# Performance work log

Hardware: AMD Instinct MI355X
Metric: run time of the kernel (lower is better)

## Reference

```python
import jax, jax.numpy as jnp
import numpy as np
import math

B, S, D, H = 4, 2048, 1024, 16
DEPTH = D // H


def setup_inputs() -> dict:
    key = jax.random.key(0)
    ks = jax.random.split(key, 8)
    scale = 1.0 / math.sqrt(D)
    return {
        "v": jax.random.normal(ks[0], (B, S, D), dtype=jnp.float32),
        "k": jax.random.normal(ks[1], (B, S, D), dtype=jnp.float32),
        "q": jax.random.normal(ks[2], (B, S, D), dtype=jnp.float32),
        "wq_w": jax.random.normal(ks[3], (D, D), dtype=jnp.float32) * scale,
        "wq_b": jnp.zeros((D,), dtype=jnp.float32),
        "wk_w": jax.random.normal(ks[4], (D, D), dtype=jnp.float32) * scale,
        "wk_b": jnp.zeros((D,), dtype=jnp.float32),
        "wv_w": jax.random.normal(ks[5], (D, D), dtype=jnp.float32) * scale,
        "wv_b": jnp.zeros((D,), dtype=jnp.float32),
        "dense_w": jax.random.normal(ks[6], (D, D), dtype=jnp.float32) * scale,
        "dense_b": jnp.zeros((D,), dtype=jnp.float32),
    }


def _split_heads(x):
    # [B, S, D] -> [B, H, S, depth]
    b, s, _ = x.shape
    return x.reshape(b, s, H, DEPTH).transpose(0, 2, 1, 3)


def reference(v, k, q, wq_w, wq_b, wk_w, wk_b, wv_w, wv_b, dense_w, dense_b):
    # Linear projections (torch Linear: x @ W.T + b)
    qh = _split_heads(q @ wq_w.T + wq_b)
    kh = _split_heads(k @ wk_w.T + wk_b)
    vh = _split_heads(v @ wv_w.T + wv_b)

    # scaled dot-product attention; scores: [B, H, S, S]
    scores = jnp.einsum("bhqd,bhkd->bhqk", qh, kh) / math.sqrt(DEPTH)
    attn = jax.nn.softmax(scores, axis=-1)
    ctx = jnp.einsum("bhqk,bhkd->bhqd", attn, vh)

    # merge heads: [B, H, S, depth] -> [B, S, D]
    ctx = ctx.transpose(0, 2, 1, 3).reshape(q.shape[0], -1, D)
    return ctx @ dense_w.T + dense_b
```

## Files before the change

### kernel.cpp

```cpp
#include <hip/hip_runtime.h>
#include <hip/hip_bf16.h>
#include <stdint.h>

#define B_  4
#define S_  2048
#define D_  1024
#define H_  16
#define DP_ 64
#define M_  (B_*S_)

typedef __bf16 bf16x8 __attribute__((ext_vector_type(8)));
typedef __bf16 bf16x2_t __attribute__((ext_vector_type(2)));
typedef float  f32x4  __attribute__((ext_vector_type(4)));
typedef float  f32x16 __attribute__((ext_vector_type(16)));
typedef float  f32x2_t __attribute__((ext_vector_type(2)));
typedef unsigned short u16x8 __attribute__((ext_vector_type(8)));

__device__ __forceinline__ unsigned short f2bf(float f) {
    __bf16 b = (__bf16)f;
    return __builtin_bit_cast(unsigned short, b);
}
__device__ __forceinline__ unsigned pk_bf16(float lo, float hi) {
    f32x2_t f = {lo, hi};
    bf16x2_t b = __builtin_convertvector(f, bf16x2_t);
    return __builtin_bit_cast(unsigned, b);
}
__device__ __forceinline__ bf16x8 ld_frag(const unsigned short* p) {
    return __builtin_bit_cast(bf16x8, *(const u16x8*)p);
}
__device__ __forceinline__ f32x4 mfma16(bf16x8 a, bf16x8 b, f32x4 c) {
    return __builtin_amdgcn_mfma_f32_16x16x32_bf16(a, b, c, 0, 0, 0);
}
__device__ __forceinline__ f32x16 mfma32(bf16x8 a, bf16x8 b, f32x16 c) {
    return __builtin_amdgcn_mfma_f32_32x32x16_bf16(a, b, c, 0, 0, 0);
}
__device__ __forceinline__ void pl32swap(unsigned &a, unsigned &b) {
    asm volatile("v_permlane32_swap_b32 %0, %1" : "+v"(a), "+v"(b));
}
__device__ __forceinline__ void gl2lds16(const void* g, void* l) {
    __builtin_amdgcn_global_load_lds(
        (const __attribute__((address_space(1))) unsigned*)g,
        (__attribute__((address_space(3))) unsigned*)l, 16, 0, 0);
}

__global__ __launch_bounds__(256)
void cvt_all(const float* __restrict__ w0, const float* __restrict__ w1,
             const float* __restrict__ w2, const float* __restrict__ w3,
             const float* __restrict__ a0, const float* __restrict__ a1,
             const float* __restrict__ a2,
             unsigned short* __restrict__ Wcat, unsigned short* __restrict__ Acat)
{
    const int gid = blockIdx.x * 256 + threadIdx.x;
    const float* src; unsigned short* dst;
    if (gid < 524288) {
        const int wi = gid >> 17;
        const size_t off = (size_t)(gid & 131071) * 8;
        const float* ws[4] = {w0, w1, w2, w3};
        src = ws[wi] + off; dst = Wcat + (size_t)wi * 1048576 + off;
    } else {
        const int g2 = gid - 524288;
        const int ai = g2 >> 20;
        const size_t off = (size_t)(g2 & 1048575) * 8;
        const float* as[3] = {a0, a1, a2};
        src = as[ai] + off; dst = Acat + (size_t)ai * 8388608 + off;
    }
    float4 x = ((const float4*)src)[0];
    float4 y = ((const float4*)src)[1];
    uint4 o;
    o.x = pk_bf16(x.x, x.y); o.y = pk_bf16(x.z, x.w);
    o.z = pk_bf16(y.x, y.y); o.w = pk_bf16(y.z, y.w);
    *(uint4*)dst = o;
}

template<int MODE>
__global__ __launch_bounds__(256, 3)
void gemm_bt(const unsigned short* __restrict__ Acat, size_t a_stride,
             const unsigned short* __restrict__ Wcat,
             const float* __restrict__ bias0, const float* __restrict__ bias1,
             void* __restrict__ Out)
{
    __shared__ __align__(16) unsigned short SM[16384];
    unsigned short* As = SM;
    unsigned short* Bs = SM + 8192;

    const int z = (MODE == 1) ? blockIdx.z : 0;
    const unsigned short* A = Acat + (size_t)z * a_stride;
    const unsigned short* W = Wcat + ((size_t)z << 20);
    const float* bias = (z == 0) ? bias0 : bias1;

    const int tid  = threadIdx.x;
    const int wave = tid >> 6, lane = tid & 63;
    const int quad = lane >> 4, l16 = lane & 15;
    const int wm = (wave >> 1) * 64, wn = (wave & 1) * 64;
    const int row0 = blockIdx.x * 128, col0 = blockIdx.y * 128;

    const int srow = lane >> 3;
    const int sg   = (lane & 7) ^ srow;

    f32x4 acc[4][4];
#pragma unroll
    for (int i = 0; i < 4; i++)
#pragma unroll
        for (int j = 0; j < 4; j++) acc[i][j] = (f32x4){0.f, 0.f, 0.f, 0.f};

    auto stage = [&](int kt) {
        const int k0 = kt * 64;
#pragma unroll
        for (int j = 0; j < 4; ++j) {
            const int c = wave * 4 + j;
            gl2lds16(A + (size_t)(row0 + c * 8 + srow) * D_ + k0 + sg * 8,
                     (unsigned char*)As + c * 1024);
            gl2lds16(W + (size_t)(col0 + c * 8 + srow) * D_ + k0 + sg * 8,
                     (unsigned char*)Bs + c * 1024);
        }
    };

    stage(0);
    for (int kt = 0; kt < D_ / 64; ++kt) {
        __syncthreads();
        bf16x8 af[4][2], bv[4][2];
#pragma unroll
        for (int mi = 0; mi < 4; ++mi) {
            const int row = wm + mi * 16 + l16;
#pragma unroll
            for (int kd = 0; kd < 2; ++kd)
                af[mi][kd] = ld_frag(&As[row * 64 + (((kd * 4 + quad) ^ (row & 7)) * 8)]);
        }
#pragma unroll
        for (int ni = 0; ni < 4; ++ni) {
            const int row = wn + ni * 16 + l16;
#pragma unroll
            for (int kd = 0; kd < 2; ++kd)
                bv[ni][kd] = ld_frag(&Bs[row * 64 + (((kd * 4 + quad) ^ (row & 7)) * 8)]);
        }
        if (kt + 1 < D_ / 64) {
            __syncthreads();
            stage(kt + 1);
        }
#pragma unroll
        for (int kd = 0; kd < 2; ++kd)
#pragma unroll
            for (int mi = 0; mi < 4; ++mi)
#pragma unroll
                for (int ni = 0; ni < 4; ++ni) {
                    if (MODE == 1)
                        acc[mi][ni] = mfma16(bv[ni][kd], af[mi][kd], acc[mi][ni]);
                    else
                        acc[mi][ni] = mfma16(af[mi][kd], bv[ni][kd], acc[mi][ni]);
                }
    }

    if constexpr (MODE == 1) {
        unsigned short* Lt = SM;
        unsigned short* OutQK = (unsigned short*)Out + ((size_t)z << 23);
        const int bidx = row0 >> 11;
        const float scale = (z == 0) ? 0.18033688f : 1.0f;
#pragma unroll
        for (int hc = 0; hc < 2; ++hc) {
            __syncthreads();
            if ((wave & 1) == hc) {
#pragma unroll
                for (int ni = 0; ni < 4; ++ni) {
                    const int c_loc = wn + ni * 16 + quad * 4;
                    const float4 bb = *(const float4*)&bias[col0 + c_loc];
#pragma unroll
                    for (int mi = 0; mi < 4; ++mi) {
                        const int s_loc = wm + mi * 16 + l16;
                        uint2 w;
                        w.x = pk_bf16((acc[mi][ni][0] + bb.x) * scale,
                                      (acc[mi][ni][1] + bb.y) * scale);
                        w.y = pk_bf16((acc[mi][ni][2] + bb.z) * scale,
                                      (acc[mi][ni][3] + bb.w) * scale);
                        *(uint2*)&Lt[s_loc * 72 + (c_loc & 63)] = w;
                    }
                }
            }
            __syncthreads();
            const int hg = (col0 >> 6) + hc;
            const size_t qb = (size_t)(bidx * H_ + hg) * S_ + (row0 & (S_ - 1));
#pragma unroll
            for (int p = 0; p < 4; ++p) {
                const int s = p * 32 + (tid >> 3);
                const int g = tid & 7;
                uint4 d = *(const uint4*)&Lt[s * 72 + g * 8];
                *(uint4*)(OutQK + (qb + s) * DP_ + g * 8) = d;
            }
        }
        return;
    }
    if constexpr (MODE == 2) {
        unsigned short* Lt = SM;
        unsigned short* OutV = (unsigned short*)Out;
        const int bidx = row0 >> 11;
#pragma unroll
        for (int hc = 0; hc < 2; ++hc) {
            __syncthreads();
            if ((wave & 1) == hc) {
#pragma unroll
                for (int ni = 0; ni < 4; ++ni) {
                    const float bvv = bias0[col0 + hc * 64 + ni * 16 + l16];
#pragma unroll
                    for (int mi = 0; mi < 4; ++mi) {
                        uint2 w;
                        w.x = pk_bf16(acc[mi][ni][0] + bvv, acc[mi][ni][1] + bvv);
                        w.y = pk_bf16(acc[mi][ni][2] + bvv, acc[mi][ni][3] + bvv);
                        *(uint2*)&Lt[(ni * 16 + l16) * 132 + wm + mi * 16 + quad * 4] = w;
                    }
                }
            }
            __syncthreads();
            const int hg = (col0 >> 6) + hc;
            const size_t vb = ((size_t)(bidx * H_ + hg) * DP_) * S_;
#pragma unroll
            for (int p = 0; p < 4; ++p) {
                const int dpl = p * 16 + (tid >> 4);
                uint4 d = *(const uint4*)&Lt[dpl * 132 + (tid & 15) * 8];
                *(uint4*)(OutV + vb + (size_t)dpl * S_ + (row0 & (S_ - 1)) + (tid & 15) * 8) = d;
            }
        }
        return;
    }
#pragma unroll
    for (int ni = 0; ni < 4; ni++) {
        const int col = col0 + wn + ni * 16 + l16;
        const float bvv = bias0[col];
#pragma unroll
        for (int mi = 0; mi < 4; mi++) {
            const int rowb = row0 + wm + mi * 16 + quad * 4;
#pragma unroll
            for (int r = 0; r < 4; r++)
                ((float*)Out)[(size_t)(rowb + r) * D_ + col] = acc[mi][ni][r] + bvv;
        }
    }
}

__global__ __launch_bounds__(256)
void flash_attn(const unsigned short* __restrict__ Qh,
                const unsigned short* __restrict__ Kh,
                const unsigned short* __restrict__ Vtg,
                unsigned short* __restrict__ Ctx)
{
    __shared__ __align__(16) unsigned short Kt[128 * 64];
    __shared__ __align__(16) unsigned short Vt[2][64 * 128];

    const int tid  = threadIdx.x;
    const int wave = tid >> 6, lane = tid & 63;
    const int l32 = lane & 31, hi = lane >> 5;
    const int bh = blockIdx.x, qt = blockIdx.y;
    const size_t base = (size_t)bh * S_ * DP_;

    bf16x8 qf[4];
#pragma unroll
    for (int dpc = 0; dpc < 4; ++dpc)
        qf[dpc] = ld_frag(&Qh[base + (size_t)(qt * 128 + wave * 32 + l32) * DP_ + dpc * 16 + hi * 8]);

    f32x16 o[2] = {};
    f32x2_t ls = {0.f, 0.f};

    const int kswz  = ((lane & 7) ^ (lane >> 3)) * 8;
    const int vdp_l = lane >> 4;
    const int vslot = lane & 15;

    auto stageK = [&](int t) {
#pragma unroll
        for (int j = 0; j < 4; ++j) {
            const int ck = wave * 4 + j;
            gl2lds16(Kh + base + (size_t)(t * 128 + ck * 8 + (lane >> 3)) * DP_ + kswz,
                     (unsigned char*)Kt + ck * 1024);
        }
    };
    auto stageV = [&](int t, unsigned short* Vb) {
#pragma unroll
        for (int j = 0; j < 4; ++j) {
            const int ck = wave * 4 + j;
            const int dp = ck * 4 + vdp_l;
            gl2lds16(Vtg + base + (size_t)dp * S_ + t * 128 + ((vslot ^ (dp & 15)) * 8),
                     (unsigned char*)Vb + ck * 1024);
        }
    };

    stageK(0); stageV(0, Vt[0]);

    for (int t = 0; t < S_ / 128; ++t) {
        __syncthreads();

        f32x16 st[4] = {};
        __builtin_amdgcn_s_setprio(1);
#pragma unroll
        for (int kt = 0; kt < 4; ++kt) {
#pragma unroll
            for (int dpc = 0; dpc < 4; ++dpc) {
                bf16x8 kf = ld_frag(&Kt[(kt * 32 + l32) * 64 + ((((dpc << 1) + hi) ^ (l32 & 7)) * 8)]);
                st[kt] = mfma32(kf, qf[dpc], st[kt]);
            }
        }
        __builtin_amdgcn_s_setprio(0);

        __syncthreads();
        if (t + 1 < S_ / 128) {
            stageK(t + 1);
            stageV(t + 1, Vt[(t + 1) & 1]);
        }

        const unsigned short* Vc = Vt[t & 1];
#pragma unroll
        for (int kt = 0; kt < 4; ++kt) {
            float p[16];
#pragma unroll
            for (int r = 0; r < 16; ++r) p[r] = __builtin_amdgcn_exp2f(st[kt][r]);
#pragma unroll
            for (int r = 0; r < 16; r += 2) ls += (f32x2_t){p[r], p[r + 1]};
            unsigned m[8];
#pragma unroll
            for (int j = 0; j < 8; ++j) m[j] = pk_bf16(p[2 * j], p[2 * j + 1]);
            pl32swap(m[0], m[2]); pl32swap(m[1], m[3]);
            pl32swap(m[4], m[6]); pl32swap(m[5], m[7]);
            __builtin_amdgcn_s_setprio(1);
#pragma unroll
            for (int c = 0; c < 2; ++c) {
                const bf16x8 pa = __builtin_bit_cast(bf16x8,
                    (uint4){m[4 * c], m[4 * c + 1], m[4 * c + 2], m[4 * c + 3]});
#pragma unroll
                for (int nt = 0; nt < 2; ++nt) {
                    const int dp = nt * 32 + l32;
                    bf16x8 vb = ld_frag(&Vc[dp * 128 + ((((kt << 2) + (c << 1) + hi) ^ (dp & 15)) * 8)]);
                    o[nt] = mfma32(pa, vb, o[nt]);
                }
            }
            __builtin_amdgcn_s_setprio(0);
        }
    }

    float lsum = ls[0] + ls[1];
    lsum += __shfl_xor(lsum, 32, 64);
    const float inv = __builtin_amdgcn_rcpf(lsum);

    const int b = bh >> 4, h = bh & 15;
#pragma unroll
    for (int r = 0; r < 16; ++r) {
        const int qrow = (r & 3) + 8 * (r >> 2) + 4 * hi;
        const float invr = __shfl(inv, qrow, 64);
        const int s = qt * 128 + wave * 32 + qrow;
#pragma unroll
        for (int nt = 0; nt < 2; ++nt)
            Ctx[((size_t)(b * S_ + s)) * D_ + h * DP_ + nt * 32 + l32] = f2bf(o[nt][r] * invr);
    }
}

extern "C" void kernel_launch(void* const* d_in, const int* in_sizes, int n_in,
                              void* d_out, int out_size, void* d_ws, size_t ws_size,
                              hipStream_t stream)
{
    const float* v    = (const float*)d_in[0];
    const float* k    = (const float*)d_in[1];
    const float* q    = (const float*)d_in[2];
    const float* wq_w = (const float*)d_in[3];
    const float* wq_b = (const float*)d_in[4];
    const float* wk_w = (const float*)d_in[5];
    const float* wk_b = (const float*)d_in[6];
    const float* wv_w = (const float*)d_in[7];
    const float* wv_b = (const float*)d_in[8];
    const float* dw   = (const float*)d_in[9];
    const float* db   = (const float*)d_in[10];
    float* out = (float*)d_out;

    unsigned short* Qh   = (unsigned short*)d_ws;
    unsigned short* Kh   = Qh   + (size_t)M_ * D_;
    unsigned short* Vt   = Kh   + (size_t)M_ * D_;
    unsigned short* Ctx  = Vt   + (size_t)M_ * D_;
    unsigned short* Wcat = Ctx  + (size_t)M_ * D_;
    unsigned short* Acat = Wcat + (size_t)4 * D_ * D_;

    cvt_all<<<14336, 256, 0, stream>>>(wq_w, wk_w, wv_w, dw, q, k, v, Wcat, Acat);

    dim3 blk(256);
    gemm_bt<1><<<dim3(M_ / 128, D_ / 128, 2), blk, 0, stream>>>(
        Acat, (size_t)M_ * D_, Wcat, wq_b, wk_b, Qh);
    gemm_bt<2><<<dim3(M_ / 128, D_ / 128, 1), blk, 0, stream>>>(
        Acat + (size_t)2 * M_ * D_, 0, Wcat + (size_t)2 * D_ * D_, wv_b, wv_b, Vt);

    flash_attn<<<dim3(B_ * H_, S_ / 128), blk, 0, stream>>>(Qh, Kh, Vt, Ctx);

    gemm_bt<0><<<dim3(M_ / 128, D_ / 128, 1), blk, 0, stream>>>(
        Ctx, 0, Wcat + (size_t)3 * D_ * D_, db, db, out);
}
```

Measured before the change: 331.0 us.

## Merge Q/K/V projections into one launch and compute softmax row sums via MFMA

The V projection moves into the same launch as Q and K: a third grid z-slice picks the non-swapped MFMA operand order and writes the transposed V layout, so one kernel launch and one tail are removed. In flash attention, the per-lane row-sum accumulation and the final shuffle reduction are replaced by an extra MFMA that multiplies the bf16 probabilities by a ones vector, which yields row sums already laid out like the output rows. This adds one MFMA per P fragment, and the sums now come from bf16-rounded probabilities rather than fp32 values. It also removes VALU adds and cross-lane shuffles.

```diff
diff --git a/kernel.cpp b/kernel.cpp
--- a/kernel.cpp
+++ b/kernel.cpp
@@ -15,6 +15,9 @@
 typedef float  f32x16 __attribute__((ext_vector_type(16)));
 typedef float  f32x2_t __attribute__((ext_vector_type(2)));
 typedef unsigned short u16x8 __attribute__((ext_vector_type(8)));
+
+struct SwapT  { static constexpr bool v = true;  };
+struct NoSwapT{ static constexpr bool v = false; };
 
 __device__ __forceinline__ unsigned short f2bf(float f) {
     __bf16 b = (__bf16)f;
@@ -77,7 +80,8 @@
 void gemm_bt(const unsigned short* __restrict__ Acat, size_t a_stride,
              const unsigned short* __restrict__ Wcat,
              const float* __restrict__ bias0, const float* __restrict__ bias1,
-             void* __restrict__ Out)
+             const float* __restrict__ bias2,
+             void* __restrict__ Out, void* __restrict__ Out2)
 {
     __shared__ __align__(16) unsigned short SM[16384];
     unsigned short* As = SM;
@@ -86,7 +90,7 @@
     const int z = (MODE == 1) ? blockIdx.z : 0;
     const unsigned short* A = Acat + (size_t)z * a_stride;
     const unsigned short* W = Wcat + ((size_t)z << 20);
-    const float* bias = (z == 0) ? bias0 : bias1;
+    const float* bias = (z == 0) ? bias0 : (z == 1 ? bias1 : bias2);
 
     const int tid  = threadIdx.x;
     const int wave = tid >> 6, lane = tid & 63;
@@ -115,107 +119,112 @@
         }
     };
 
-    stage(0);
-    for (int kt = 0; kt < D_ / 64; ++kt) {
-        __syncthreads();
-        bf16x8 af[4][2], bv[4][2];
-#pragma unroll
-        for (int mi = 0; mi < 4; ++mi) {
-            const int row = wm + mi * 16 + l16;
+    auto kloop = [&](auto tag) {
+        constexpr bool SW = decltype(tag)::v;
+        stage(0);
+        for (int kt = 0; kt < D_ / 64; ++kt) {
+            __syncthreads();
+            bf16x8 af[4][2], bv[4][2];
+#pragma unroll
+            for (int mi = 0; mi < 4; ++mi) {
+                const int row = wm + mi * 16 + l16;
+#pragma unroll
+                for (int kd = 0; kd < 2; ++kd)
+                    af[mi][kd] = ld_frag(&As[row * 64 + (((kd * 4 + quad) ^ (row & 7)) * 8)]);
+            }
+#pragma unroll
+            for (int ni = 0; ni < 4; ++ni) {
+                const int row = wn + ni * 16 + l16;
+#pragma unroll
+                for (int kd = 0; kd < 2; ++kd)
+                    bv[ni][kd] = ld_frag(&Bs[row * 64 + (((kd * 4 + quad) ^ (row & 7)) * 8)]);
+            }
+            if (kt + 1 < D_ / 64) {
+                __syncthreads();
+                stage(kt + 1);
+            }
 #pragma unroll
             for (int kd = 0; kd < 2; ++kd)
-                af[mi][kd] = ld_frag(&As[row * 64 + (((kd * 4 + quad) ^ (row & 7)) * 8)]);
-        }
-#pragma unroll
-        for (int ni = 0; ni < 4; ++ni) {
-            const int row = wn + ni * 16 + l16;
-#pragma unroll
-            for (int kd = 0; kd < 2; ++kd)
-                bv[ni][kd] = ld_frag(&Bs[row * 64 + (((kd * 4 + quad) ^ (row & 7)) * 8)]);
-        }
-        if (kt + 1 < D_ / 64) {
-            __syncthreads();
-            stage(kt + 1);
-        }
-#pragma unroll
-        for (int kd = 0; kd < 2; ++kd)
-#pragma unroll
-            for (int mi = 0; mi < 4; ++mi)
-#pragma unroll
-                for (int ni = 0; ni < 4; ++ni) {
-                    if (MODE == 1)
-                        acc[mi][ni] = mfma16(bv[ni][kd], af[mi][kd], acc[mi][ni]);
-                    else
-                        acc[mi][ni] = mfma16(af[mi][kd], bv[ni][kd], acc[mi][ni]);
-                }
-    }
+#pragma unroll
+                for (int mi = 0; mi < 4; ++mi)
+#pragma unroll
+                    for (int ni = 0; ni < 4; ++ni) {
+                        if constexpr (SW)
+                            acc[mi][ni] = mfma16(bv[ni][kd], af[mi][kd], acc[mi][ni]);
+                        else
+                            acc[mi][ni] = mfma16(af[mi][kd], bv[ni][kd], acc[mi][ni]);
+                    }
+        }
+    };
+    if (MODE == 1 && z < 2) kloop(SwapT{});
+    else                    kloop(NoSwapT{});
 
     if constexpr (MODE == 1) {
-        unsigned short* Lt = SM;
-        unsigned short* OutQK = (unsigned short*)Out + ((size_t)z << 23);
-        const int bidx = row0 >> 11;
-        const float scale = (z == 0) ? 0.18033688f : 1.0f;
-#pragma unroll
-        for (int hc = 0; hc < 2; ++hc) {
-            __syncthreads();
-            if ((wave & 1) == hc) {
-#pragma unroll
-                for (int ni = 0; ni < 4; ++ni) {
-                    const int c_loc = wn + ni * 16 + quad * 4;
-                    const float4 bb = *(const float4*)&bias[col0 + c_loc];
-#pragma unroll
-                    for (int mi = 0; mi < 4; ++mi) {
-                        const int s_loc = wm + mi * 16 + l16;
-                        uint2 w;
-                        w.x = pk_bf16((acc[mi][ni][0] + bb.x) * scale,
-                                      (acc[mi][ni][1] + bb.y) * scale);
-                        w.y = pk_bf16((acc[mi][ni][2] + bb.z) * scale,
-                                      (acc[mi][ni][3] + bb.w) * scale);
-                        *(uint2*)&Lt[s_loc * 72 + (c_loc & 63)] = w;
+        if (z < 2) {
+            unsigned short* Lt = SM;
+            unsigned short* OutQK = (unsigned short*)Out + ((size_t)z << 23);
+            const int bidx = row0 >> 11;
+            const float scale = (z == 0) ? 0.18033688f : 1.0f;
+#pragma unroll
+            for (int hc = 0; hc < 2; ++hc) {
+                __syncthreads();
+                if ((wave & 1) == hc) {
+#pragma unroll
+                    for (int ni = 0; ni < 4; ++ni) {
+                        const int c_loc = wn + ni * 16 + quad * 4;
+                        const float4 bb = *(const float4*)&bias[col0 + c_loc];
+#pragma unroll
+                        for (int mi = 0; mi < 4; ++mi) {
+                            const int s_loc = wm + mi * 16 + l16;
+                            uint2 w;
+                            w.x = pk_bf16((acc[mi][ni][0] + bb.x) * scale,
+                                          (acc[mi][ni][1] + bb.y) * scale);
+                            w.y = pk_bf16((acc[mi][ni][2] + bb.z) * scale,
+                                          (acc[mi][ni][3] + bb.w) * scale);
+                            *(uint2*)&Lt[s_loc * 72 + (c_loc & 63)] = w;
+                        }
                     }
                 }
-            }
-            __syncthreads();
-            const int hg = (col0 >> 6) + hc;
-            const size_t qb = (size_t)(bidx * H_ + hg) * S_ + (row0 & (S_ - 1));
-#pragma unroll
-            for (int p = 0; p < 4; ++p) {
-                const int s = p * 32 + (tid >> 3);
-                const int g = tid & 7;
-                uint4 d = *(const uint4*)&Lt[s * 72 + g * 8];
-                *(uint4*)(OutQK + (qb + s) * DP_ + g * 8) = d;
-            }
-        }
-        return;
-    }
-    if constexpr (MODE == 2) {
-        unsigned short* Lt = SM;
-        unsigned short* OutV = (unsigned short*)Out;
-        const int bidx = row0 >> 11;
-#pragma unroll
-        for (int hc = 0; hc < 2; ++hc) {
-            __syncthreads();
-            if ((wave & 1) == hc) {
-#pragma unroll
-                for (int ni = 0; ni < 4; ++ni) {
-                    const float bvv = bias0[col0 + hc * 64 + ni * 16 + l16];
-#pragma unroll
-                    for (int mi = 0; mi < 4; ++mi) {
-                        uint2 w;
-                        w.x = pk_bf16(acc[mi][ni][0] + bvv, acc[mi][ni][1] + bvv);
-                        w.y = pk_bf16(acc[mi][ni][2] + bvv, acc[mi][ni][3] + bvv);
-                        *(uint2*)&Lt[(ni * 16 + l16) * 132 + wm + mi * 16 + quad * 4] = w;
+                __syncthreads();
+                const int hg = (col0 >> 6) + hc;
+                const size_t qb = (size_t)(bidx * H_ + hg) * S_ + (row0 & (S_ - 1));
+#pragma unroll
+                for (int p = 0; p < 4; ++p) {
+                    const int s = p * 32 + (tid >> 3);
+                    const int g = tid & 7;
+                    uint4 d = *(const uint4*)&Lt[s * 72 + g * 8];
+                    *(uint4*)(OutQK + (qb + s) * DP_ + g * 8) = d;
+                }
+            }
+        } else {
+            unsigned short* Lt = SM;
+            unsigned short* OutV = (unsigned short*)Out2;
+            const int bidx = row0 >> 11;
+#pragma unroll
+            for (int hc = 0; hc < 2; ++hc) {
+                __syncthreads();
+                if ((wave & 1) == hc) {
+#pragma unroll
+                    for (int ni = 0; ni < 4; ++ni) {
+                        const float bvv = bias[col0 + hc * 64 + ni * 16 + l16];
+#pragma unroll
+                        for (int mi = 0; mi < 4; ++mi) {
+                            uint2 w;
+                            w.x = pk_bf16(acc[mi][ni][0] + bvv, acc[mi][ni][1] + bvv);
+                            w.y = pk_bf16(acc[mi][ni][2] + bvv, acc[mi][ni][3] + bvv);
+                            *(uint2*)&Lt[(ni * 16 + l16) * 132 + wm + mi * 16 + quad * 4] = w;
+                        }
                     }
                 }
-            }
-            __syncthreads();
-            const int hg = (col0 >> 6) + hc;
-            const size_t vb = ((size_t)(bidx * H_ + hg) * DP_) * S_;
-#pragma unroll
-            for (int p = 0; p < 4; ++p) {
-                const int dpl = p * 16 + (tid >> 4);
-                uint4 d = *(const uint4*)&Lt[dpl * 132 + (tid & 15) * 8];
-                *(uint4*)(OutV + vb + (size_t)dpl * S_ + (row0 & (S_ - 1)) + (tid & 15) * 8) = d;
+                __syncthreads();
+                const int hg = (col0 >> 6) + hc;
+                const size_t vb = ((size_t)(bidx * H_ + hg) * DP_) * S_;
+#pragma unroll
+                for (int p = 0; p < 4; ++p) {
+                    const int dpl = p * 16 + (tid >> 4);
+                    uint4 d = *(const uint4*)&Lt[dpl * 132 + (tid & 15) * 8];
+                    *(uint4*)(OutV + vb + (size_t)dpl * S_ + (row0 & (S_ - 1)) + (tid & 15) * 8) = d;
+                }
             }
         }
         return;
@@ -255,7 +264,10 @@
         qf[dpc] = ld_frag(&Qh[base + (size_t)(qt * 128 + wave * 32 + l32) * DP_ + dpc * 16 + hi * 8]);
 
     f32x16 o[2] = {};
-    f32x2_t ls = {0.f, 0.f};
+    f32x16 lsacc = {};
+    bf16x8 onesf;
+#pragma unroll
+    for (int j = 0; j < 8; ++j) onesf[j] = (__bf16)1.0f;
 
     const int kswz  = ((lane & 7) ^ (lane >> 3)) * 8;
     const int vdp_l = lane >> 4;
@@ -308,8 +320,6 @@
             float p[16];
 #pragma unroll
             for (int r = 0; r < 16; ++r) p[r] = __builtin_amdgcn_exp2f(st[kt][r]);
-#pragma unroll
-            for (int r = 0; r < 16; r += 2) ls += (f32x2_t){p[r], p[r + 1]};
             unsigned m[8];
 #pragma unroll
             for (int j = 0; j < 8; ++j) m[j] = pk_bf16(p[2 * j], p[2 * j + 1]);
@@ -320,6 +330,7 @@
             for (int c = 0; c < 2; ++c) {
                 const bf16x8 pa = __builtin_bit_cast(bf16x8,
                     (uint4){m[4 * c], m[4 * c + 1], m[4 * c + 2], m[4 * c + 3]});
+                lsacc = mfma32(pa, onesf, lsacc);
 #pragma unroll
                 for (int nt = 0; nt < 2; ++nt) {
                     const int dp = nt * 32 + l32;
@@ -331,15 +342,11 @@
         }
     }
 
-    float lsum = ls[0] + ls[1];
-    lsum += __shfl_xor(lsum, 32, 64);
-    const float inv = __builtin_amdgcn_rcpf(lsum);
-
     const int b = bh >> 4, h = bh & 15;
 #pragma unroll
     for (int r = 0; r < 16; ++r) {
         const int qrow = (r & 3) + 8 * (r >> 2) + 4 * hi;
-        const float invr = __shfl(inv, qrow, 64);
+        const float invr = __builtin_amdgcn_rcpf(lsacc[r]);
         const int s = qt * 128 + wave * 32 + qrow;
 #pragma unroll
         for (int nt = 0; nt < 2; ++nt)
@@ -374,13 +381,11 @@
     cvt_all<<<14336, 256, 0, stream>>>(wq_w, wk_w, wv_w, dw, q, k, v, Wcat, Acat);
 
     dim3 blk(256);
-    gemm_bt<1><<<dim3(M_ / 128, D_ / 128, 2), blk, 0, stream>>>(
-        Acat, (size_t)M_ * D_, Wcat, wq_b, wk_b, Qh);
-    gemm_bt<2><<<dim3(M_ / 128, D_ / 128, 1), blk, 0, stream>>>(
-        Acat + (size_t)2 * M_ * D_, 0, Wcat + (size_t)2 * D_ * D_, wv_b, wv_b, Vt);
+    gemm_bt<1><<<dim3(M_ / 128, D_ / 128, 3), blk, 0, stream>>>(
+        Acat, (size_t)M_ * D_, Wcat, wq_b, wk_b, wv_b, Qh, Vt);
 
     flash_attn<<<dim3(B_ * H_, S_ / 128), blk, 0, stream>>>(Qh, Kh, Vt, Ctx);
 
     gemm_bt<0><<<dim3(M_ / 128, D_ / 128, 1), blk, 0, stream>>>(
-        Ctx, 0, Wcat + (size_t)3 * D_ * D_, db, db, out);
-}
+        Ctx, 0, Wcat + (size_t)3 * D_ * D_, db, db, db, out, nullptr);
+}
```

Measured after the change: 331.3 us. About the same (+0.1%).
